# Kernel tuning notes

Hardware: AMD Instinct MI355X
Metric: run time of the kernel (lower is better)

## Reference

```python
import jax, jax.numpy as jnp
import numpy as np

EPS_RMS = 1e-6
EPS_SCALE = 1e-5


def setup_inputs() -> dict:
    key = jax.random.key(0)
    k1, k2 = jax.random.split(key)
    B, S, D_IN, D_OUT = 4, 2048, 2048, 8192
    x = jax.random.normal(k1, (B, S, D_IN), dtype=jnp.float32)
    # kaiming_uniform-ish init bound
    bound = 1.0 / np.sqrt(D_IN)
    weight = jax.random.uniform(k2, (D_OUT, D_IN), dtype=jnp.float32, minval=-bound, maxval=bound)
    gamma = jnp.ones((D_IN,), dtype=jnp.float32)
    return {"x": x, "weight": weight, "gamma": gamma}


def rmsnorm(x, gamma):
    xf = x.astype(jnp.float32)
    inv = jax.lax.rsqrt(jnp.mean(xf * xf, axis=-1, keepdims=True) + EPS_RMS)
    return (xf * inv).astype(x.dtype) * gamma


def quantize_weights_ternary(weight):
    scale = jnp.maximum(jnp.mean(jnp.abs(weight)), EPS_SCALE)
    wn = weight / scale
    wq = jax.lax.stop_gradient(jnp.round(jnp.clip(wn, -1.0, 1.0)) - wn) + wn  # STE
    return wq, scale


def reference(x, weight, gamma):
    x_norm = rmsnorm(x, gamma)                      # [B, S, D_in]
    wq, scale = quantize_weights_ternary(weight)    # [D_out, D_in], scalar
    out = jnp.einsum('bsd,od->bso', x_norm, wq)     # [B, S, D_out]
    return out * scale
```

## Files before the change

### kernel.cpp

```cpp
#include <hip/hip_runtime.h>
#include <hip/hip_bf16.h>
#include <stdint.h>

#define M_ROWS 8192
#define K_DIM  2048
#define N_DIM  8192
#define W_ELEMS (N_DIM * K_DIM)
#define X_ELEMS (M_ROWS * K_DIM)
#define NT 32
#define ABSUM_BLOCKS 256

typedef __bf16 v8bf __attribute__((ext_vector_type(8)));
typedef float  v4f  __attribute__((ext_vector_type(4)));

__device__ inline unsigned short f2bf(float f) {
  uint32_t u = __builtin_bit_cast(uint32_t, f);
  uint32_t r = (u + 0x7fffu + ((u >> 16) & 1u)) >> 16;
  return (unsigned short)r;
}

__device__ inline void async_copy16(const void* g, void* l) {
  __builtin_amdgcn_global_load_lds(
      (const __attribute__((address_space(1))) void*)g,
      (__attribute__((address_space(3))) void*)l, 16, 0, 0);
}

__device__ inline float scale_from_partials(const double* __restrict__ partials) {
  const int lane = threadIdx.x & 63;
  double d = partials[lane] + partials[lane + 64] +
             partials[lane + 128] + partials[lane + 192];
  for (int off = 32; off > 0; off >>= 1) d += __shfl_down(d, off);
  d = __shfl(d, 0);
  return (float)fmax(d * (1.0 / (double)W_ELEMS), 1e-5);
}

__global__ __launch_bounds__(256) void prep_kernel(const float* __restrict__ X,
                                                   const float* __restrict__ gamma,
                                                   const float* __restrict__ W,
                                                   unsigned short* __restrict__ Xn,
                                                   double* __restrict__ partials) {
  __shared__ double wsumd[4];
  __shared__ float wsumf[4];
  const int t = threadIdx.x;
  const int lane = t & 63, wid = t >> 6;

  if (blockIdx.x < ABSUM_BLOCKS) {
    const int pb = blockIdx.x;
    int tid = pb * 256 + t;
    const float4* W4 = (const float4*)W;
    const int n4 = W_ELEMS / 4;
    double acc = 0.0;
    for (int i = tid; i < n4; i += ABSUM_BLOCKS * 256) {
      float4 v = W4[i];
      acc += (double)fabsf(v.x) + (double)fabsf(v.y) +
             (double)fabsf(v.z) + (double)fabsf(v.w);
    }
    for (int off = 32; off > 0; off >>= 1) acc += __shfl_down(acc, off);
    if (lane == 0) wsumd[wid] = acc;
    __syncthreads();
    if (t == 0) partials[pb] = wsumd[0] + wsumd[1] + wsumd[2] + wsumd[3];
    return;
  }

  const int row = blockIdx.x - ABSUM_BLOCKS;
  const float4* xr = (const float4*)(X + (size_t)row * K_DIM);
  float4 a = xr[t];
  float4 b = xr[t + 256];
  float ss = a.x * a.x + a.y * a.y + a.z * a.z + a.w * a.w +
             b.x * b.x + b.y * b.y + b.z * b.z + b.w * b.w;
  for (int off = 32; off > 0; off >>= 1) ss += __shfl_down(ss, off);
  if (lane == 0) wsumf[wid] = ss;
  __syncthreads();
  float total = wsumf[0] + wsumf[1] + wsumf[2] + wsumf[3];
  float inv = 1.0f / sqrtf(total * (1.0f / (float)K_DIM) + 1e-6f);
  const float4* gr = (const float4*)gamma;
  float4 g0 = gr[t];
  float4 g1 = gr[t + 256];
  union { unsigned short h[4]; uint2 u; } pa, pb;
  pa.h[0] = f2bf((a.x * inv) * g0.x);
  pa.h[1] = f2bf((a.y * inv) * g0.y);
  pa.h[2] = f2bf((a.z * inv) * g0.z);
  pa.h[3] = f2bf((a.w * inv) * g0.w);
  pb.h[0] = f2bf((b.x * inv) * g1.x);
  pb.h[1] = f2bf((b.y * inv) * g1.y);
  pb.h[2] = f2bf((b.z * inv) * g1.z);
  pb.h[3] = f2bf((b.w * inv) * g1.w);
  uint2* orow = (uint2*)(Xn + (size_t)row * K_DIM);
  orow[t] = pa.u;
  orow[t + 256] = pb.u;
}

__global__ __launch_bounds__(256) void quant_kernel(const float* __restrict__ W,
                                                    const double* __restrict__ partials,
                                                    float* __restrict__ scale_out,
                                                    unsigned short* __restrict__ Wq) {
  const float s = scale_from_partials(partials);
  const int t = threadIdx.x;
  if (blockIdx.x == 0 && t == 0) scale_out[0] = s;
  const float4* W4 = (const float4*)W + (size_t)blockIdx.x * 512;
  float4 a = W4[t];
  float4 b = W4[t + 256];
  union { unsigned short h[4]; uint2 u; } pa, pb;
  pa.h[0] = f2bf(rintf(fminf(1.f, fmaxf(-1.f, a.x / s))));
  pa.h[1] = f2bf(rintf(fminf(1.f, fmaxf(-1.f, a.y / s))));
  pa.h[2] = f2bf(rintf(fminf(1.f, fmaxf(-1.f, a.z / s))));
  pa.h[3] = f2bf(rintf(fminf(1.f, fmaxf(-1.f, a.w / s))));
  pb.h[0] = f2bf(rintf(fminf(1.f, fmaxf(-1.f, b.x / s))));
  pb.h[1] = f2bf(rintf(fminf(1.f, fmaxf(-1.f, b.y / s))));
  pb.h[2] = f2bf(rintf(fminf(1.f, fmaxf(-1.f, b.z / s))));
  pb.h[3] = f2bf(rintf(fminf(1.f, fmaxf(-1.f, b.w / s))));
  uint2* o = (uint2*)(Wq + (size_t)blockIdx.x * 2048);
  o[t] = pa.u;
  o[t + 256] = pb.u;
}

__global__ __launch_bounds__(512, 2) void gemm_kernel(
    const unsigned short* __restrict__ A,
    const unsigned short* __restrict__ B,
    const float* __restrict__ scale,
    float* __restrict__ C) {
  __shared__ __align__(16) char lds[131072];

  const int tid = threadIdx.x;
  const int lane = tid & 63;
  const int wave = tid >> 6;
  const int wm = wave & 1;
  const int wn = wave >> 1;

  const int bid = blockIdx.x;
  const int swz = (bid & 7) * 128 + (bid >> 3);
  const int st = swz >> 4, wi = swz & 15;
  const int mb = (st >> 3) * 4 + (wi >> 2);
  const int nb = (st & 7) * 4 + (wi & 3);
  const int m0 = mb * 256;
  const int n0 = nb * 256;

  const int srow3 = lane >> 3;
  const int scg = (lane & 7) ^ srow3;

  const int aoff_a = wm * 8192 + (lane & 15) * 128;
  const int boff_b = wn * 4096 + (lane & 15) * 128;
  const int swzk0 = ((lane >> 4) ^ (lane & 7)) << 4;
  const int swzk1 = ((4 + (lane >> 4)) ^ (lane & 7)) << 4;

  v4f acc[8][4] = {};
  v8bf af[4][2];
  v8bf b0f[2][2];
  v8bf b1f[2][2];

#define STAGE_A(B_, H_, KT_) do {                                              \
    _Pragma("unroll")                                                          \
    for (int j = 0; j < 2; ++j) {                                              \
      const int chunk_ = wave * 2 + j;                                         \
      const int slot_ = chunk_ * 8 + srow3;                                    \
      const int row_ = ((slot_ >> 6) << 7) + ((H_) << 6) + (slot_ & 63);       \
      async_copy16(A + (size_t)(m0 + row_) * K_DIM + ((KT_) << 6) + (scg << 3),\
                   lds + (B_) * 32768 + (H_) * 16384 + chunk_ * 1024);         \
    } } while (0)

#define STAGE_B(B_, H_, KT_) do {                                              \
    _Pragma("unroll")                                                          \
    for (int j = 0; j < 2; ++j) {                                              \
      const int chunk_ = wave * 2 + j;                                         \
      const int slot_ = chunk_ * 8 + srow3;                                    \
      const int row_ = ((slot_ >> 5) << 6) + ((H_) << 5) + (slot_ & 31);       \
      async_copy16(B + (size_t)(n0 + row_) * K_DIM + ((KT_) << 6) + (scg << 3),\
                   lds + 65536 + (B_) * 32768 + (H_) * 16384 + chunk_ * 1024); \
    } } while (0)

#define LOADA(B_, QM_) do {                                                    \
    _Pragma("unroll")                                                          \
    for (int tm = 0; tm < 4; ++tm) {                                           \
      af[tm][0] = *(const v8bf*)(lds + (B_) * 32768 + (QM_) * 16384 +          \
                                 aoff_a + tm * 2048 + swzk0);                  \
      af[tm][1] = *(const v8bf*)(lds + (B_) * 32768 + (QM_) * 16384 +          \
                                 aoff_a + tm * 2048 + swzk1);                  \
    } } while (0)

#define LOADB(B_, QN_, DST) do {                                               \
    _Pragma("unroll")                                                          \
    for (int tn = 0; tn < 2; ++tn) {                                           \
      DST[tn][0] = *(const v8bf*)(lds + 65536 + (B_) * 32768 + (QN_) * 16384 + \
                                  boff_b + tn * 2048 + swzk0);                 \
      DST[tn][1] = *(const v8bf*)(lds + 65536 + (B_) * 32768 + (QN_) * 16384 + \
                                  boff_b + tn * 2048 + swzk1);                 \
    } } while (0)

#define MMAC(BF, QM_, QN_) do {                                                \
    _Pragma("unroll")                                                          \
    for (int ks = 0; ks < 2; ++ks)                                             \
    _Pragma("unroll")                                                          \
    for (int tm = 0; tm < 4; ++tm)                                             \
    _Pragma("unroll")                                                          \
    for (int tn = 0; tn < 2; ++tn)                                             \
      acc[(QM_) * 4 + tm][(QN_) * 2 + tn] =                                    \
          __builtin_amdgcn_mfma_f32_16x16x32_bf16(                             \
              BF[tn][ks], af[tm][ks],                                          \
              acc[(QM_) * 4 + tm][(QN_) * 2 + tn], 0, 0, 0);                   \
  } while (0)

#define SYNC8() do {                                                           \
    asm volatile("s_waitcnt vmcnt(8)" ::: "memory");                           \
    __builtin_amdgcn_s_barrier();                                              \
    asm volatile("" ::: "memory");                                             \
    __builtin_amdgcn_sched_barrier(0);                                         \
  } while (0)

#define TILE(T_, B_) do {                                                      \
    const int t1_ = ((T_) + 1 < NT) ? (T_) + 1 : NT - 1;                       \
    const int t2_ = ((T_) + 2 < NT) ? (T_) + 2 : NT - 1;                       \
                                  \
    LOADA(B_, 0);                                                              \
    STAGE_A(1 - (B_), 1, t1_);                                                 \
    __builtin_amdgcn_s_setprio(1); MMAC(b0f, 0, 0);                            \
    __builtin_amdgcn_s_setprio(0);                                             \
                                                            \
    LOADB(B_, 1, b1f);                                                         \
    __builtin_amdgcn_s_setprio(1); MMAC(b1f, 0, 1);                            \
    __builtin_amdgcn_s_setprio(0);                                             \
    SYNC8();                                                                   \
                                                            \
    LOADA(B_, 1);                                                              \
    STAGE_A(B_, 0, t2_);                                                       \
    STAGE_B(B_, 1, t2_);                                                       \
    __builtin_amdgcn_s_setprio(1); MMAC(b0f, 1, 0);                            \
    __builtin_amdgcn_s_setprio(0);                                             \
                                                            \
    STAGE_B(B_, 0, t2_);                                                       \
    __builtin_amdgcn_s_setprio(1); MMAC(b1f, 1, 1);                            \
    __builtin_amdgcn_s_setprio(0);                                             \
    SYNC8();                                                                   \
    LOADB(1 - (B_), 0, b0f);                                                   \
  } while (0)

  STAGE_A(0, 0, 0);
  STAGE_B(0, 0, 0);
  STAGE_B(0, 1, 0);
  STAGE_A(0, 1, 0);
  STAGE_A(1, 0, 1);
  STAGE_B(1, 1, 1);
  STAGE_B(1, 0, 1);
  SYNC8();
  LOADB(0, 0, b0f);

  for (int t = 0; t < NT; t += 2) {
    TILE(t, 0);
    TILE(t + 1, 1);
  }

  const float s = scale[0];
  const int mBase = m0 + wm * 128 + (lane & 15);
  const int nBase = n0 + wn * 64 + ((lane >> 4) << 2);
#pragma unroll
  for (int tm = 0; tm < 8; ++tm) {
#pragma unroll
    for (int tn = 0; tn < 4; ++tn) {
      float4 v;
      v.x = acc[tm][tn][0] * s;
      v.y = acc[tm][tn][1] * s;
      v.z = acc[tm][tn][2] * s;
      v.w = acc[tm][tn][3] * s;
      *(float4*)&C[(size_t)(mBase + tm * 16) * N_DIM + (nBase + tn * 16)] = v;
    }
  }

#undef STAGE_A
#undef STAGE_B
#undef LOADA
#undef LOADB
#undef MMAC
#undef SYNC8
#undef TILE
}

extern "C" void kernel_launch(void* const* d_in, const int* in_sizes, int n_in,
                              void* d_out, int out_size, void* d_ws, size_t ws_size,
                              hipStream_t stream) {
  const float* x = (const float*)d_in[0];
  const float* w = (const float*)d_in[1];
  const float* gamma = (const float*)d_in[2];
  float* out = (float*)d_out;

  float* scale_f = (float*)d_ws;
  unsigned short* xn = (unsigned short*)((char*)d_ws + 16);
  unsigned short* wq = (unsigned short*)((char*)d_ws + 16 + (size_t)X_ELEMS * 2);
  double* partials = (double*)out;

  prep_kernel<<<ABSUM_BLOCKS + M_ROWS, 256, 0, stream>>>(x, gamma, w, xn, partials);
  quant_kernel<<<W_ELEMS / 2048, 256, 0, stream>>>(w, partials, scale_f, wq);
  gemm_kernel<<<(M_ROWS / 256) * (N_DIM / 256), 512, 0, stream>>>(xn, wq, scale_f, out);
}
```

Baseline: 611.2 us.

## Restructure GEMM main loop into four barrier-separated phases with finer prefetch

Rewrites the per-tile pipeline of the ternary GEMM into four uniform phases. Each phase reads LDS fragments, issues one async global-to-LDS stage for the next tiles, runs one quarter of the MFMAs, and then waits on vmcnt(6) before a barrier. Stages are spread more evenly across the tile and the prologue issues fewer tiles ahead. The aim is better overlap of global loads, LDS reads and MFMA work, at the cost of twice as many barriers per tile and a shallower prefetch lead.

```diff
diff --git a/kernel.cpp b/kernel.cpp
--- a/kernel.cpp
+++ b/kernel.cpp
@@ -199,48 +199,35 @@
               acc[(QM_) * 4 + tm][(QN_) * 2 + tn], 0, 0, 0);                   \
   } while (0)
 
-#define SYNC8() do {                                                           \
-    asm volatile("s_waitcnt vmcnt(8)" ::: "memory");                           \
-    __builtin_amdgcn_s_barrier();                                              \
-    asm volatile("" ::: "memory");                                             \
-    __builtin_amdgcn_sched_barrier(0);                                         \
+#define BAR()    __builtin_amdgcn_s_barrier()
+#define SCHED0() __builtin_amdgcn_sched_barrier(0)
+#define VMG6()   asm volatile("s_waitcnt vmcnt(6)" ::: "memory")
+
+#define PHASE(READS_, STAGE_, MM_) do {                                        \
+    READS_;                                                                    \
+    STAGE_;                                                                    \
+    BAR();                                                                     \
+    __builtin_amdgcn_s_setprio(1); MM_;                                        \
+    __builtin_amdgcn_s_setprio(0);                                             \
+    VMG6(); BAR(); SCHED0();                                                   \
   } while (0)
 
 #define TILE(T_, B_) do {                                                      \
     const int t1_ = ((T_) + 1 < NT) ? (T_) + 1 : NT - 1;                       \
     const int t2_ = ((T_) + 2 < NT) ? (T_) + 2 : NT - 1;                       \
-                                  \
-    LOADA(B_, 0);                                                              \
-    STAGE_A(1 - (B_), 1, t1_);                                                 \
-    __builtin_amdgcn_s_setprio(1); MMAC(b0f, 0, 0);                            \
-    __builtin_amdgcn_s_setprio(0);                                             \
-                                                            \
-    LOADB(B_, 1, b1f);                                                         \
-    __builtin_amdgcn_s_setprio(1); MMAC(b1f, 0, 1);                            \
-    __builtin_amdgcn_s_setprio(0);                                             \
-    SYNC8();                                                                   \
-                                                            \
-    LOADA(B_, 1);                                                              \
-    STAGE_A(B_, 0, t2_);                                                       \
-    STAGE_B(B_, 1, t2_);                                                       \
-    __builtin_amdgcn_s_setprio(1); MMAC(b0f, 1, 0);                            \
-    __builtin_amdgcn_s_setprio(0);                                             \
-                                                            \
-    STAGE_B(B_, 0, t2_);                                                       \
-    __builtin_amdgcn_s_setprio(1); MMAC(b1f, 1, 1);                            \
-    __builtin_amdgcn_s_setprio(0);                                             \
-    SYNC8();                                                                   \
-    LOADB(1 - (B_), 0, b0f);                                                   \
+    PHASE(LOADA(B_, 0),            STAGE_A(1 - (B_), 0, t1_), MMAC(b0f, 0, 0));\
+    PHASE(LOADB(B_, 1, b1f),       STAGE_B(1 - (B_), 1, t1_), MMAC(b1f, 0, 1));\
+    PHASE(LOADA(B_, 1),            STAGE_A(1 - (B_), 1, t1_), MMAC(b0f, 1, 0));\
+    PHASE(LOADB(1 - (B_), 0, b0f), STAGE_B(B_, 0, t2_),       MMAC(b1f, 1, 1));\
   } while (0)
 
+  STAGE_B(0, 0, 0);
   STAGE_A(0, 0, 0);
-  STAGE_B(0, 0, 0);
   STAGE_B(0, 1, 0);
   STAGE_A(0, 1, 0);
-  STAGE_A(1, 0, 1);
-  STAGE_B(1, 1, 1);
   STAGE_B(1, 0, 1);
-  SYNC8();
+  VMG6();
+  BAR(); SCHED0();
   LOADB(0, 0, b0f);
 
   for (int t = 0; t < NT; t += 2) {
@@ -269,7 +256,10 @@
 #undef LOADA
 #undef LOADB
 #undef MMAC
-#undef SYNC8
+#undef BAR
+#undef SCHED0
+#undef VMG6
+#undef PHASE
 #undef TILE
 }
 
```

Measured after the change: 598.9 us. 1.02x faster.
